# Kernel tuning notes

Measured on AMD Instinct MI355X. Metric: run time of the kernel, lower is better.

Reference implementation:

```python
import jax, jax.numpy as jnp
import numpy as np
from jax import lax


def setup_inputs() -> dict:
    key = jax.random.key(0)
    k1, k2 = jax.random.split(key)
    N, dim, m = 8192, 1024, 1024
    x = jax.random.normal(k1, (N, dim), dtype=jnp.float32)
    vectors = jax.random.normal(k2, (m, dim), dtype=jnp.float32) * 0.01
    bias = jnp.zeros((dim,), dtype=jnp.float32)
    return {"x": x, "vectors": vectors, "bias": bias}


def reference(x, vectors, bias):
    # Normalize each reflection vector to unit length: [m, d]
    v_normed = vectors / jnp.linalg.norm(vectors, axis=1, keepdims=True)

    def step(out, v):
        # out: [N, d], v: [d]
        proj = out @ v                       # [N]
        out = out - 2.0 * proj[:, None] * v  # rank-1 Householder update
        return out, None

    out, _ = lax.scan(step, x, v_normed)
    return out + bias
```

## Files before the change

### kernel.cpp

```cpp
#include <hip/hip_runtime.h>
#include <hip/hip_bf16.h>

typedef __attribute__((ext_vector_type(8))) short short8;
typedef __attribute__((ext_vector_type(4))) short s16x4;
typedef __attribute__((ext_vector_type(4))) float f32x4;

static __device__ inline short f2bf(float f) {
    unsigned u = __float_as_uint(f);
    unsigned r = (u + 0x7fffu + ((u >> 16) & 1u)) >> 16;
    return (short)r;
}
static __device__ inline float bf2f(short h) {
    return __uint_as_float(((unsigned)(unsigned short)h) << 16);
}

static __device__ inline int swz32(int row, int slot) {
    return row * 32 + ((slot ^ ((row >> 1) & 3)) << 3);
}
static __device__ inline int swz64(int row, int slot) {
    return row * 64 + ((slot ^ (row & 7)) << 3);
}

__global__ __launch_bounds__(256) void k_normalize(const float* __restrict__ vec,
                                                   float* __restrict__ V, int dim) {
    int row = blockIdx.x;
    const float4* src = (const float4*)(vec + (size_t)row * dim);
    float4* dst = (float4*)(V + (size_t)row * dim);
    int nv4 = dim >> 2;
    float ss = 0.f;
    for (int i = threadIdx.x; i < nv4; i += blockDim.x) {
        float4 v = src[i];
        ss += v.x * v.x + v.y * v.y + v.z * v.z + v.w * v.w;
    }
    for (int off = 32; off; off >>= 1) ss += __shfl_down(ss, off, 64);
    __shared__ float ws_[4];
    int lane = threadIdx.x & 63, w = threadIdx.x >> 6;
    if (lane == 0) ws_[w] = ss;
    __syncthreads();
    float inv = 1.0f / sqrtf(ws_[0] + ws_[1] + ws_[2] + ws_[3]);
    for (int i = threadIdx.x; i < nv4; i += blockDim.x) {
        float4 v = src[i];
        v.x *= inv; v.y *= inv; v.z *= inv; v.w *= inv;
        dst[i] = v;
    }
}

__global__ __launch_bounds__(256) void k_split(const float* __restrict__ X,
                                               short* __restrict__ Xh,
                                               short* __restrict__ Xl, int n4) {
    for (int i = blockIdx.x * blockDim.x + threadIdx.x; i < n4; i += gridDim.x * blockDim.x) {
        float4 v = ((const float4*)X)[i];
        float f[4] = {v.x, v.y, v.z, v.w};
        s16x4 h, l;
#pragma unroll
        for (int q = 0; q < 4; ++q) {
            h[q] = f2bf(f[q]);
            l[q] = f2bf(f[q] - bf2f(h[q]));
        }
        *(s16x4*)&Xh[(size_t)i * 4] = h;
        *(s16x4*)&Xl[(size_t)i * 4] = l;
    }
}

__global__ __launch_bounds__(256) void k_cast(const float* __restrict__ X,
                                              short* __restrict__ Xh, int n4) {
    for (int i = blockIdx.x * blockDim.x + threadIdx.x; i < n4; i += gridDim.x * blockDim.x) {
        float4 v = ((const float4*)X)[i];
        float f[4] = {v.x, v.y, v.z, v.w};
        s16x4 h;
#pragma unroll
        for (int q = 0; q < 4; ++q) h[q] = f2bf(f[q]);
        *(s16x4*)&Xh[(size_t)i * 4] = h;
    }
}

__global__ __launch_bounds__(256) void k_tsplit(const float* __restrict__ X,
                                                short* __restrict__ Xth,
                                                short* __restrict__ Xtl, int R, int C) {
    __shared__ float tile[32][33];
    int c0 = blockIdx.x * 32, r0 = blockIdx.y * 32;
    int t = threadIdx.x;
    int r = t >> 3, c4 = (t & 7) * 4;
    float4 v = *(const float4*)&X[(size_t)(r0 + r) * C + c0 + c4];
    tile[r][c4 + 0] = v.x; tile[r][c4 + 1] = v.y;
    tile[r][c4 + 2] = v.z; tile[r][c4 + 3] = v.w;
    __syncthreads();
    int rr = t >> 3, cc4 = (t & 7) * 4;
    s16x4 h, l;
#pragma unroll
    for (int q = 0; q < 4; ++q) {
        float f = tile[cc4 + q][rr];
        h[q] = f2bf(f);
        l[q] = f2bf(f - bf2f(h[q]));
    }
    *(s16x4*)&Xth[(size_t)(c0 + rr) * R + r0 + cc4] = h;
    *(s16x4*)&Xtl[(size_t)(c0 + rr) * R + r0 + cc4] = l;
}

template<int MODE, int TRI>
__global__ __launch_bounds__(256) void k_nt64(
    const short* __restrict__ Ah, const short* __restrict__ Al,
    const short* __restrict__ Bh, const short* __restrict__ Bl,
    float* __restrict__ Cf, short* __restrict__ Ch, short* __restrict__ Cl,
    int K, int lda, int ldb, int ldc) {
    __shared__ short As[2][64 * 32];
    __shared__ short Bs[2][64 * 32];
    int i0 = blockIdx.y * 64, j0 = blockIdx.x * 64;
    if (TRI == 2 && j0 < i0) return;
    int KE = (TRI == 1) ? (j0 + 64) : K;
    int t = threadIdx.x, lane = t & 63, wave = t >> 6;
    int wr = wave >> 1, wc = wave & 1;
    int srow = t >> 2, slot = t & 3;
    int sofs = swz32(srow, slot);
    int gofs = slot * 8;
    f32x4 acc[2][2] = {};
    for (int k0 = 0; k0 < KE; k0 += 32) {
        __syncthreads();
        *(short8*)&As[0][sofs] = *(const short8*)&Ah[(size_t)(i0 + srow) * lda + k0 + gofs];
        *(short8*)&As[1][sofs] = *(const short8*)&Al[(size_t)(i0 + srow) * lda + k0 + gofs];
        *(short8*)&Bs[0][sofs] = *(const short8*)&Bh[(size_t)(j0 + srow) * ldb + k0 + gofs];
        *(short8*)&Bs[1][sofs] = *(const short8*)&Bl[(size_t)(j0 + srow) * ldb + k0 + gofs];
        __syncthreads();
        int g = lane >> 4;
        short8 ah[2], al2[2], bh[2], bl2[2];
#pragma unroll
        for (int i = 0; i < 2; ++i) {
            int ro = swz32(wr * 32 + i * 16 + (lane & 15), g);
            ah[i] = *(const short8*)&As[0][ro];
            al2[i] = *(const short8*)&As[1][ro];
        }
#pragma unroll
        for (int j = 0; j < 2; ++j) {
            int ro = swz32(wc * 32 + j * 16 + (lane & 15), g);
            bh[j] = *(const short8*)&Bs[0][ro];
            bl2[j] = *(const short8*)&Bs[1][ro];
        }
#pragma unroll
        for (int i = 0; i < 2; ++i)
#pragma unroll
            for (int j = 0; j < 2; ++j) {
                acc[i][j] = __builtin_amdgcn_mfma_f32_16x16x32_bf16(ah[i], bh[j], acc[i][j], 0, 0, 0);
                acc[i][j] = __builtin_amdgcn_mfma_f32_16x16x32_bf16(ah[i], bl2[j], acc[i][j], 0, 0, 0);
                acc[i][j] = __builtin_amdgcn_mfma_f32_16x16x32_bf16(al2[i], bh[j], acc[i][j], 0, 0, 0);
            }
    }
#pragma unroll
    for (int i = 0; i < 2; ++i)
#pragma unroll
        for (int j = 0; j < 2; ++j) {
            int row0 = i0 + wr * 32 + i * 16 + ((lane >> 4) << 2);
            int col = j0 + wc * 32 + j * 16 + (lane & 15);
#pragma unroll
            for (int r = 0; r < 4; ++r) {
                float v = acc[i][j][r];
                size_t idx = (size_t)(row0 + r) * ldc + col;
                if (MODE == 2) {
                    Ch[idx] = f2bf((((row0 + r) == col) ? 1.f : 0.f) - v);
                } else {
                    short h = f2bf(v);
                    short l = f2bf(v - bf2f(h));
                    Ch[idx] = h;
                    Cl[idx] = l;
                    if (MODE == 3) Cf[idx] = v;
                }
            }
        }
}

__global__ __launch_bounds__(256) void k_baseinv2(const float* __restrict__ G,
                                                  short* __restrict__ Th, short* __restrict__ Tl,
                                                  short* __restrict__ Tth, short* __restrict__ Ttl,
                                                  int m) {
    __shared__ float Rs[64 * 64];
    int d = blockIdx.x >> 4, g = blockIdx.x & 15;
    int b0 = d * 64;
    int t = threadIdx.x, lane = t & 63, wave = t >> 6;
    {
        int r = t >> 2, c00 = (t & 3) * 16;
#pragma unroll
        for (int q = 0; q < 4; ++q)
            *(float4*)&Rs[r * 64 + c00 + q * 4] =
                *(const float4*)&G[(size_t)(b0 + r) * m + b0 + c00 + q * 4];
    }
    __syncthreads();
    int c = g * 4 + wave;
    float x = 0.f;
    for (int r = c; r >= 0; --r) {
        float prod = Rs[r * 64 + lane] * x;
        float s = prod;
#pragma unroll
        for (int off = 32; off; off >>= 1) s += __shfl_xor(s, off, 64);
        if (lane == r) x = ((r == c) ? 2.f : 0.f) - 2.f * s;
    }
    short h = f2bf(x);
    short l = f2bf(x - bf2f(h));
    Th[(size_t)(b0 + lane) * m + b0 + c] = h;
    Tl[(size_t)(b0 + lane) * m + b0 + c] = l;
    Tth[(size_t)(b0 + c) * m + b0 + lane] = h;
    Ttl[(size_t)(b0 + c) * m + b0 + lane] = l;
}

template<int PHASE>
__global__ __launch_bounds__(256) void k_trimm(
    const short* __restrict__ Ah, const short* __restrict__ Al,
    const short* __restrict__ Bh, const short* __restrict__ Bl,
    short* __restrict__ C1h, short* __restrict__ C1l,
    short* __restrict__ C2h, short* __restrict__ C2l,
    int m, int s) {
    __shared__ short As[2][64 * 32];
    __shared__ short Bs[2][64 * 32];
    int p = blockIdx.z;
    int a0 = 2 * p * s, c0 = a0 + s;
    int r0 = blockIdx.y * 64, ct = blockIdx.x * 64;
    int KS = (PHASE == 1) ? 0 : r0;
    int KE = (PHASE == 1) ? (ct + 64) : s;
    size_t tbase = (size_t)p * s * s;
    int t = threadIdx.x, lane = t & 63, wave = t >> 6;
    int wr = wave >> 1, wc = wave & 1;
    int srow = t >> 2, slot = t & 3;
    int sofs = swz32(srow, slot);
    int gofs = slot * 8;
    f32x4 acc[2][2] = {};
    for (int k0 = KS; k0 < KE; k0 += 32) {
        __syncthreads();
        if (PHASE == 1) {
            *(short8*)&As[0][sofs] = *(const short8*)&Ah[(size_t)(a0 + r0 + srow) * m + c0 + k0 + gofs];
            *(short8*)&As[1][sofs] = *(const short8*)&Al[(size_t)(a0 + r0 + srow) * m + c0 + k0 + gofs];
            *(short8*)&Bs[0][sofs] = *(const short8*)&Bh[(size_t)(c0 + ct + srow) * m + c0 + k0 + gofs];
            *(short8*)&Bs[1][sofs] = *(const short8*)&Bl[(size_t)(c0 + ct + srow) * m + c0 + k0 + gofs];
        } else {
            *(short8*)&As[0][sofs] = *(const short8*)&Ah[(size_t)(a0 + r0 + srow) * m + a0 + k0 + gofs];
            *(short8*)&As[1][sofs] = *(const short8*)&Al[(size_t)(a0 + r0 + srow) * m + a0 + k0 + gofs];
            *(short8*)&Bs[0][sofs] = *(const short8*)&Bh[tbase + (size_t)(ct + srow) * s + k0 + gofs];
            *(short8*)&Bs[1][sofs] = *(const short8*)&Bl[tbase + (size_t)(ct + srow) * s + k0 + gofs];
        }
        __syncthreads();
        int g = lane >> 4;
        short8 ah[2], al2[2], bh[2], bl2[2];
#pragma unroll
        for (int i = 0; i < 2; ++i) {
            int ro = swz32(wr * 32 + i * 16 + (lane & 15), g);
            ah[i] = *(const short8*)&As[0][ro];
            al2[i] = *(const short8*)&As[1][ro];
        }
#pragma unroll
        for (int j = 0; j < 2; ++j) {
            int ro = swz32(wc * 32 + j * 16 + (lane & 15), g);
            bh[j] = *(const short8*)&Bs[0][ro];
            bl2[j] = *(const short8*)&Bs[1][ro];
        }
#pragma unroll
        for (int i = 0; i < 2; ++i)
#pragma unroll
            for (int j = 0; j < 2; ++j) {
                acc[i][j] = __builtin_amdgcn_mfma_f32_16x16x32_bf16(ah[i], bh[j], acc[i][j], 0, 0, 0);
                acc[i][j] = __builtin_amdgcn_mfma_f32_16x16x32_bf16(ah[i], bl2[j], acc[i][j], 0, 0, 0);
                acc[i][j] = __builtin_amdgcn_mfma_f32_16x16x32_bf16(al2[i], bh[j], acc[i][j], 0, 0, 0);
            }
    }
#pragma unroll
    for (int i = 0; i < 2; ++i)
#pragma unroll
        for (int j = 0; j < 2; ++j) {
            int row0 = r0 + wr * 32 + i * 16 + ((lane >> 4) << 2);
            int col = ct + wc * 32 + j * 16 + (lane & 15);
#pragma unroll
            for (int r = 0; r < 4; ++r) {
                if (PHASE == 1) {
                    float v = acc[i][j][r];
                    short h = f2bf(v);
                    short l = f2bf(v - bf2f(h));
                    size_t idx = tbase + (size_t)col * s + row0 + r;
                    C1h[idx] = h;
                    C1l[idx] = l;
                } else {
                    float v = -acc[i][j][r];
                    short h = f2bf(v);
                    short l = f2bf(v - bf2f(h));
                    int R = a0 + row0 + r, Cc = c0 + col;
                    C1h[(size_t)R * m + Cc] = h;
                    C1l[(size_t)R * m + Cc] = l;
                    C2h[(size_t)Cc * m + R] = h;
                    C2l[(size_t)Cc * m + R] = l;
                }
            }
        }
}

__global__ __launch_bounds__(256) void k_apply3(const short* __restrict__ xh,
                                                const short* __restrict__ Qt,
                                                const float* __restrict__ bias,
                                                float* __restrict__ out, int dim) {
    __shared__ short As[128 * 64];
    __shared__ short Bs[128 * 64];
    int m0 = blockIdx.y * 128, n0 = blockIdx.x * 128;
    int t = threadIdx.x, lane = t & 63, wave = t >> 6;
    int wr = wave >> 1, wc = wave & 1;
    int sr = lane >> 3;
    int sslot = (lane & 7) ^ (sr & 7);
    f32x4 acc[4][4] = {};
    for (int k0 = 0; k0 < dim; k0 += 64) {
        __syncthreads();
#pragma unroll
        for (int q = 0; q < 4; ++q) {
            int rg = wave * 4 + q;
            int row = rg * 8 + sr;
            const short* gA = &xh[(size_t)(m0 + row) * dim + k0 + sslot * 8];
            const short* gB = &Qt[(size_t)(n0 + row) * dim + k0 + sslot * 8];
            __builtin_amdgcn_global_load_lds(
                (const __attribute__((address_space(1))) void*)gA,
                (__attribute__((address_space(3))) void*)&As[rg * 8 * 64], 16, 0, 0);
            __builtin_amdgcn_global_load_lds(
                (const __attribute__((address_space(1))) void*)gB,
                (__attribute__((address_space(3))) void*)&Bs[rg * 8 * 64], 16, 0, 0);
        }
        __syncthreads();
#pragma unroll
        for (int kk = 0; kk < 2; ++kk) {
            int g = kk * 4 + (lane >> 4);
            short8 af[4], bf_[4];
#pragma unroll
            for (int i = 0; i < 4; ++i)
                af[i] = *(const short8*)&As[swz64(wr * 64 + i * 16 + (lane & 15), g)];
#pragma unroll
            for (int j = 0; j < 4; ++j)
                bf_[j] = *(const short8*)&Bs[swz64(wc * 64 + j * 16 + (lane & 15), g)];
#pragma unroll
            for (int i = 0; i < 4; ++i)
#pragma unroll
                for (int j = 0; j < 4; ++j)
                    acc[i][j] = __builtin_amdgcn_mfma_f32_16x16x32_bf16(af[i], bf_[j], acc[i][j], 0, 0, 0);
        }
    }
#pragma unroll
    for (int i = 0; i < 4; ++i)
#pragma unroll
        for (int j = 0; j < 4; ++j) {
            int row = m0 + wr * 64 + i * 16 + (lane >> 4) * 4;
            int col = n0 + wc * 64 + j * 16 + (lane & 15);
            float b = bias[col];
#pragma unroll
            for (int r = 0; r < 4; ++r)
                out[(size_t)(row + r) * dim + col] = acc[i][j][r] + b;
        }
}

extern "C" void kernel_launch(void* const* d_in, const int* in_sizes, int n_in,
                              void* d_out, int out_size, void* d_ws, size_t ws_size,
                              hipStream_t stream) {
    const float* x = (const float*)d_in[0];
    const float* vec = (const float*)d_in[1];
    const float* bias = (const float*)d_in[2];
    float* out = (float*)d_out;

    int dim = in_sizes[2];
    int m = in_sizes[1] / dim;
    int n = in_sizes[0] / dim;

    const size_t MD = (size_t)m * dim;
    const size_t MM = (size_t)m * m;

    char* cur = (char*)d_ws;
    auto alloc_f = [&](size_t nelem) { float* p = (float*)cur; cur += nelem * 4; return p; };
    auto alloc_s = [&](size_t nelem) { short* p = (short*)cur; cur += nelem * 2; return p; };
    float* V   = alloc_f(MD);
    float* G   = alloc_f(MM);
    short* Vh  = alloc_s(MD);
    short* Vl  = alloc_s(MD);
    short* Vth = alloc_s(MD);
    short* Vtl = alloc_s(MD);
    short* Gh  = alloc_s(MM);
    short* Gl  = alloc_s(MM);
    short* Th  = alloc_s(MM);
    short* Tl  = alloc_s(MM);
    short* Tth = alloc_s(MM);
    short* Ttl = alloc_s(MM);
    short* Wh  = alloc_s(MD);
    short* Wl  = alloc_s(MD);
    short* Qt  = alloc_s((size_t)dim * dim);
    short* tmph = alloc_s(MM / 2);
    short* tmpl = alloc_s(MM / 2);
    short* xh  = alloc_s((size_t)n * dim);

    k_normalize<<<m, 256, 0, stream>>>(vec, V, dim);
    k_split<<<1024, 256, 0, stream>>>(V, Vh, Vl, (int)(MD / 4));
    k_tsplit<<<dim3(dim / 32, m / 32), 256, 0, stream>>>(V, Vth, Vtl, m, dim);

    k_nt64<3, 2><<<dim3(m / 64, m / 64), 256, 0, stream>>>(Vh, Vl, Vh, Vl, G, Gh, Gl,
                                                           dim, dim, dim, m);
    k_baseinv2<<<(m / 64) * 16, 256, 0, stream>>>(G, Th, Tl, Tth, Ttl, m);
    for (int s = 64; s < m; s <<= 1) {
        dim3 g(s / 64, s / 64, m / (2 * s));
        k_trimm<1><<<g, 256, 0, stream>>>(Gh, Gl, Tth, Ttl, tmph, tmpl, nullptr, nullptr, m, s);
        k_trimm<2><<<g, 256, 0, stream>>>(Th, Tl, tmph, tmpl, Th, Tl, Tth, Ttl, m, s);
    }

    k_nt64<1, 1><<<dim3(m / 64, dim / 64), 256, 0, stream>>>(Vth, Vtl, Tth, Ttl, nullptr, Wh, Wl,
                                                             m, m, m, m);
    k_nt64<2, 0><<<dim3(dim / 64, dim / 64), 256, 0, stream>>>(Vth, Vtl, Wh, Wl, nullptr, Qt, nullptr,
                                                               m, m, m, dim);

    k_cast<<<2048, 256, 0, stream>>>(x, xh, (int)((size_t)n * dim / 4));
    k_apply3<<<dim3(dim / 128, n / 128), 256, 0, stream>>>(xh, Qt, bias, out, dim);
}
```

Baseline: 178.9 us.

## Fuse prep kernels, double-buffer GEMM loads, add fused tree level, swizzle apply grid

Merges normalize, split and transposed split into one prep kernel. The small GEMM and the final apply GEMM become double-buffered, using global_load_lds prefetch of the next K tile with explicit waitcnt and barriers. A new fp32 kernel computes the first level of the triangular-inverse tree in one launch, replacing two trimm launches. The apply grid is remapped in a chunked order for cache locality. The aim is to cut launch overhead and memory stalls, at the cost of more LDS and fragile manual waitcnt counts.

```diff
diff --git a/kernel.cpp b/kernel.cpp
--- a/kernel.cpp
+++ b/kernel.cpp
@@ -21,44 +21,57 @@
     return row * 64 + ((slot ^ (row & 7)) << 3);
 }
 
-__global__ __launch_bounds__(256) void k_normalize(const float* __restrict__ vec,
-                                                   float* __restrict__ V, int dim) {
-    int row = blockIdx.x;
-    const float4* src = (const float4*)(vec + (size_t)row * dim);
-    float4* dst = (float4*)(V + (size_t)row * dim);
-    int nv4 = dim >> 2;
+__global__ __launch_bounds__(256) void k_prep(const float* __restrict__ vec,
+                                              short* __restrict__ Vh, short* __restrict__ Vl,
+                                              short* __restrict__ Vth, short* __restrict__ Vtl,
+                                              int m, int dim) {
+    __shared__ float ps[32][9];
+    __shared__ float invs[32];
+    __shared__ float tile[32][33];
+    int r0 = blockIdx.x * 32;
+    int t = threadIdx.x;
+    int r = t >> 3, seg = t & 7;
+    const float* src = vec + (size_t)(r0 + r) * dim + seg * 128;
     float ss = 0.f;
-    for (int i = threadIdx.x; i < nv4; i += blockDim.x) {
-        float4 v = src[i];
+#pragma unroll 8
+    for (int i = 0; i < 32; ++i) {
+        float4 v = *(const float4*)&src[i * 4];
         ss += v.x * v.x + v.y * v.y + v.z * v.z + v.w * v.w;
     }
-    for (int off = 32; off; off >>= 1) ss += __shfl_down(ss, off, 64);
-    __shared__ float ws_[4];
-    int lane = threadIdx.x & 63, w = threadIdx.x >> 6;
-    if (lane == 0) ws_[w] = ss;
+    ps[r][seg] = ss;
     __syncthreads();
-    float inv = 1.0f / sqrtf(ws_[0] + ws_[1] + ws_[2] + ws_[3]);
-    for (int i = threadIdx.x; i < nv4; i += blockDim.x) {
-        float4 v = src[i];
-        v.x *= inv; v.y *= inv; v.z *= inv; v.w *= inv;
-        dst[i] = v;
-    }
-}
-
-__global__ __launch_bounds__(256) void k_split(const float* __restrict__ X,
-                                               short* __restrict__ Xh,
-                                               short* __restrict__ Xl, int n4) {
-    for (int i = blockIdx.x * blockDim.x + threadIdx.x; i < n4; i += gridDim.x * blockDim.x) {
-        float4 v = ((const float4*)X)[i];
-        float f[4] = {v.x, v.y, v.z, v.w};
+    if (t < 32) {
+        float s = 0.f;
+#pragma unroll
+        for (int q = 0; q < 8; ++q) s += ps[t][q];
+        invs[t] = 1.0f / sqrtf(s);
+    }
+    __syncthreads();
+    float inv = invs[r];
+    int c4 = (t & 7) * 4;
+    for (int ct = 0; ct < dim / 32; ++ct) {
+        float4 v = *(const float4*)&vec[(size_t)(r0 + r) * dim + ct * 32 + c4];
+        float f[4] = {v.x * inv, v.y * inv, v.z * inv, v.w * inv};
         s16x4 h, l;
 #pragma unroll
         for (int q = 0; q < 4; ++q) {
             h[q] = f2bf(f[q]);
             l[q] = f2bf(f[q] - bf2f(h[q]));
-        }
-        *(s16x4*)&Xh[(size_t)i * 4] = h;
-        *(s16x4*)&Xl[(size_t)i * 4] = l;
+            tile[r][c4 + q] = f[q];
+        }
+        *(s16x4*)&Vh[(size_t)(r0 + r) * dim + ct * 32 + c4] = h;
+        *(s16x4*)&Vl[(size_t)(r0 + r) * dim + ct * 32 + c4] = l;
+        __syncthreads();
+        s16x4 th, tl;
+#pragma unroll
+        for (int q = 0; q < 4; ++q) {
+            float ff = tile[c4 + q][r];
+            th[q] = f2bf(ff);
+            tl[q] = f2bf(ff - bf2f(th[q]));
+        }
+        *(s16x4*)&Vth[(size_t)(ct * 32 + r) * m + r0 + c4] = th;
+        *(s16x4*)&Vtl[(size_t)(ct * 32 + r) * m + r0 + c4] = tl;
+        __syncthreads();
     }
 }
 
@@ -74,66 +87,61 @@
     }
 }
 
-__global__ __launch_bounds__(256) void k_tsplit(const float* __restrict__ X,
-                                                short* __restrict__ Xth,
-                                                short* __restrict__ Xtl, int R, int C) {
-    __shared__ float tile[32][33];
-    int c0 = blockIdx.x * 32, r0 = blockIdx.y * 32;
-    int t = threadIdx.x;
-    int r = t >> 3, c4 = (t & 7) * 4;
-    float4 v = *(const float4*)&X[(size_t)(r0 + r) * C + c0 + c4];
-    tile[r][c4 + 0] = v.x; tile[r][c4 + 1] = v.y;
-    tile[r][c4 + 2] = v.z; tile[r][c4 + 3] = v.w;
-    __syncthreads();
-    int rr = t >> 3, cc4 = (t & 7) * 4;
-    s16x4 h, l;
-#pragma unroll
-    for (int q = 0; q < 4; ++q) {
-        float f = tile[cc4 + q][rr];
-        h[q] = f2bf(f);
-        l[q] = f2bf(f - bf2f(h[q]));
-    }
-    *(s16x4*)&Xth[(size_t)(c0 + rr) * R + r0 + cc4] = h;
-    *(s16x4*)&Xtl[(size_t)(c0 + rr) * R + r0 + cc4] = l;
-}
-
 template<int MODE, int TRI>
-__global__ __launch_bounds__(256) void k_nt64(
+__global__ __launch_bounds__(256) void k_nt64g(
     const short* __restrict__ Ah, const short* __restrict__ Al,
     const short* __restrict__ Bh, const short* __restrict__ Bl,
     float* __restrict__ Cf, short* __restrict__ Ch, short* __restrict__ Cl,
     int K, int lda, int ldb, int ldc) {
-    __shared__ short As[2][64 * 32];
-    __shared__ short Bs[2][64 * 32];
+    __shared__ short As[2][2][64 * 32];
+    __shared__ short Bs[2][2][64 * 32];
     int i0 = blockIdx.y * 64, j0 = blockIdx.x * 64;
     if (TRI == 2 && j0 < i0) return;
     int KE = (TRI == 1) ? (j0 + 64) : K;
     int t = threadIdx.x, lane = t & 63, wave = t >> 6;
     int wr = wave >> 1, wc = wave & 1;
-    int srow = t >> 2, slot = t & 3;
-    int sofs = swz32(srow, slot);
-    int gofs = slot * 8;
+    int srow = wave * 16 + (lane >> 2);
+    int sslot = (lane & 3) ^ ((lane >> 3) & 3);
+    const short* gAh = &Ah[(size_t)(i0 + srow) * lda + sslot * 8];
+    const short* gAl = &Al[(size_t)(i0 + srow) * lda + sslot * 8];
+    const short* gBh = &Bh[(size_t)(j0 + srow) * ldb + sslot * 8];
+    const short* gBl = &Bl[(size_t)(j0 + srow) * ldb + sslot * 8];
+    auto stage = [&](int buf, int k0) {
+        __builtin_amdgcn_global_load_lds((const __attribute__((address_space(1))) void*)&gAh[k0],
+            (__attribute__((address_space(3))) void*)&As[buf][0][wave * 512], 16, 0, 0);
+        __builtin_amdgcn_global_load_lds((const __attribute__((address_space(1))) void*)&gAl[k0],
+            (__attribute__((address_space(3))) void*)&As[buf][1][wave * 512], 16, 0, 0);
+        __builtin_amdgcn_global_load_lds((const __attribute__((address_space(1))) void*)&gBh[k0],
+            (__attribute__((address_space(3))) void*)&Bs[buf][0][wave * 512], 16, 0, 0);
+        __builtin_amdgcn_global_load_lds((const __attribute__((address_space(1))) void*)&gBl[k0],
+            (__attribute__((address_space(3))) void*)&Bs[buf][1][wave * 512], 16, 0, 0);
+    };
+    int nIter = KE >> 5;
+    stage(0, 0);
     f32x4 acc[2][2] = {};
-    for (int k0 = 0; k0 < KE; k0 += 32) {
-        __syncthreads();
-        *(short8*)&As[0][sofs] = *(const short8*)&Ah[(size_t)(i0 + srow) * lda + k0 + gofs];
-        *(short8*)&As[1][sofs] = *(const short8*)&Al[(size_t)(i0 + srow) * lda + k0 + gofs];
-        *(short8*)&Bs[0][sofs] = *(const short8*)&Bh[(size_t)(j0 + srow) * ldb + k0 + gofs];
-        *(short8*)&Bs[1][sofs] = *(const short8*)&Bl[(size_t)(j0 + srow) * ldb + k0 + gofs];
-        __syncthreads();
+    for (int it = 0; it < nIter; ++it) {
+        int c = it & 1;
+        if (it + 1 < nIter) {
+            stage(c ^ 1, (it + 1) << 5);
+            asm volatile("s_waitcnt vmcnt(4)" ::: "memory");
+        } else {
+            asm volatile("s_waitcnt vmcnt(0)" ::: "memory");
+        }
+        __builtin_amdgcn_s_barrier();
+        __builtin_amdgcn_sched_barrier(0);
         int g = lane >> 4;
         short8 ah[2], al2[2], bh[2], bl2[2];
 #pragma unroll
         for (int i = 0; i < 2; ++i) {
             int ro = swz32(wr * 32 + i * 16 + (lane & 15), g);
-            ah[i] = *(const short8*)&As[0][ro];
-            al2[i] = *(const short8*)&As[1][ro];
+            ah[i] = *(const short8*)&As[c][0][ro];
+            al2[i] = *(const short8*)&As[c][1][ro];
         }
 #pragma unroll
         for (int j = 0; j < 2; ++j) {
             int ro = swz32(wc * 32 + j * 16 + (lane & 15), g);
-            bh[j] = *(const short8*)&Bs[0][ro];
-            bl2[j] = *(const short8*)&Bs[1][ro];
+            bh[j] = *(const short8*)&Bs[c][0][ro];
+            bl2[j] = *(const short8*)&Bs[c][1][ro];
         }
 #pragma unroll
         for (int i = 0; i < 2; ++i)
@@ -143,6 +151,8 @@
                 acc[i][j] = __builtin_amdgcn_mfma_f32_16x16x32_bf16(ah[i], bl2[j], acc[i][j], 0, 0, 0);
                 acc[i][j] = __builtin_amdgcn_mfma_f32_16x16x32_bf16(al2[i], bh[j], acc[i][j], 0, 0, 0);
             }
+        asm volatile("s_waitcnt lgkmcnt(0)" ::: "memory");
+        __builtin_amdgcn_s_barrier();
     }
 #pragma unroll
     for (int i = 0; i < 2; ++i)
@@ -198,6 +208,82 @@
     Tl[(size_t)(b0 + lane) * m + b0 + c] = l;
     Tth[(size_t)(b0 + c) * m + b0 + lane] = h;
     Ttl[(size_t)(b0 + c) * m + b0 + lane] = l;
+}
+
+__global__ __launch_bounds__(256) void k_tree64f(const float* __restrict__ G,
+                                                 short* __restrict__ Th, short* __restrict__ Tl,
+                                                 short* __restrict__ Tth, short* __restrict__ Ttl,
+                                                 int m) {
+    __shared__ float Gb[64 * 65];
+    __shared__ float Ai[64 * 65];
+    __shared__ float Ci[64 * 64];
+    __shared__ float Tm[64 * 64];
+    int p = blockIdx.x;
+    int a0 = p * 128, c0 = a0 + 64;
+    int t = threadIdx.x;
+    {
+        int r = t >> 2, c00 = (t & 3) * 16;
+#pragma unroll
+        for (int q = 0; q < 4; ++q) {
+            *(float4*)&Gb[r * 65 + c00 + q * 4] =
+                *(const float4*)&G[(size_t)(a0 + r) * m + c0 + c00 + q * 4];
+            s16x4 ha = *(const s16x4*)&Th[(size_t)(a0 + r) * m + a0 + c00 + q * 4];
+            s16x4 la = *(const s16x4*)&Tl[(size_t)(a0 + r) * m + a0 + c00 + q * 4];
+            s16x4 hc = *(const s16x4*)&Th[(size_t)(c0 + r) * m + c0 + c00 + q * 4];
+            s16x4 lc = *(const s16x4*)&Tl[(size_t)(c0 + r) * m + c0 + c00 + q * 4];
+#pragma unroll
+            for (int e = 0; e < 4; ++e) {
+                Ai[r * 65 + c00 + q * 4 + e] = bf2f(ha[e]) + bf2f(la[e]);
+                Ci[r * 64 + c00 + q * 4 + e] = bf2f(hc[e]) + bf2f(lc[e]);
+            }
+        }
+    }
+    __syncthreads();
+    int tx = t & 15, ty = t >> 4;
+    float acc[4][4] = {};
+#pragma unroll 4
+    for (int k = 0; k < 64; ++k) {
+        float av[4], bv[4];
+#pragma unroll
+        for (int i = 0; i < 4; ++i) av[i] = Gb[(ty * 4 + i) * 65 + k];
+#pragma unroll
+        for (int j = 0; j < 4; ++j) bv[j] = Ci[k * 64 + tx * 4 + j];
+#pragma unroll
+        for (int i = 0; i < 4; ++i)
+#pragma unroll
+            for (int j = 0; j < 4; ++j) acc[i][j] += av[i] * bv[j];
+    }
+#pragma unroll
+    for (int i = 0; i < 4; ++i)
+#pragma unroll
+        for (int j = 0; j < 4; ++j) Tm[(ty * 4 + i) * 64 + tx * 4 + j] = acc[i][j];
+    __syncthreads();
+    float acc2[4][4] = {};
+#pragma unroll 4
+    for (int k = 0; k < 64; ++k) {
+        float av[4], bv[4];
+#pragma unroll
+        for (int i = 0; i < 4; ++i) av[i] = Ai[(ty * 4 + i) * 65 + k];
+#pragma unroll
+        for (int j = 0; j < 4; ++j) bv[j] = Tm[k * 64 + tx * 4 + j];
+#pragma unroll
+        for (int i = 0; i < 4; ++i)
+#pragma unroll
+            for (int j = 0; j < 4; ++j) acc2[i][j] += av[i] * bv[j];
+    }
+#pragma unroll
+    for (int i = 0; i < 4; ++i)
+#pragma unroll
+        for (int j = 0; j < 4; ++j) {
+            float v = -acc2[i][j];
+            short h = f2bf(v);
+            short l = f2bf(v - bf2f(h));
+            int R = a0 + ty * 4 + i, C = c0 + tx * 4 + j;
+            Th[(size_t)R * m + C] = h;
+            Tl[(size_t)R * m + C] = l;
+            Tth[(size_t)C * m + R] = h;
+            Ttl[(size_t)C * m + R] = l;
+        }
 }
 
 template<int PHASE>
@@ -287,20 +373,22 @@
         }
 }
 
-__global__ __launch_bounds__(256) void k_apply3(const short* __restrict__ xh,
+__global__ __launch_bounds__(256) void k_apply4(const short* __restrict__ xh,
                                                 const short* __restrict__ Qt,
                                                 const float* __restrict__ bias,
                                                 float* __restrict__ out, int dim) {
-    __shared__ short As[128 * 64];
-    __shared__ short Bs[128 * 64];
-    int m0 = blockIdx.y * 128, n0 = blockIdx.x * 128;
+    __shared__ short As[2][128 * 64];
+    __shared__ short Bs[2][128 * 64];
+    int nwg = gridDim.x * gridDim.y;
+    int flat = blockIdx.y * gridDim.x + blockIdx.x;
+    int cpx = nwg >> 3;
+    int L = (flat & 7) * cpx + (flat >> 3);
+    int m0 = (L / gridDim.x) * 128, n0 = (L % gridDim.x) * 128;
     int t = threadIdx.x, lane = t & 63, wave = t >> 6;
     int wr = wave >> 1, wc = wave & 1;
     int sr = lane >> 3;
     int sslot = (lane & 7) ^ (sr & 7);
-    f32x4 acc[4][4] = {};
-    for (int k0 = 0; k0 < dim; k0 += 64) {
-        __syncthreads();
+    auto stage = [&](int buf, int k0) {
 #pragma unroll
         for (int q = 0; q < 4; ++q) {
             int rg = wave * 4 + q;
@@ -309,28 +397,43 @@
             const short* gB = &Qt[(size_t)(n0 + row) * dim + k0 + sslot * 8];
             __builtin_amdgcn_global_load_lds(
                 (const __attribute__((address_space(1))) void*)gA,
-                (__attribute__((address_space(3))) void*)&As[rg * 8 * 64], 16, 0, 0);
+                (__attribute__((address_space(3))) void*)&As[buf][rg * 8 * 64], 16, 0, 0);
             __builtin_amdgcn_global_load_lds(
                 (const __attribute__((address_space(1))) void*)gB,
-                (__attribute__((address_space(3))) void*)&Bs[rg * 8 * 64], 16, 0, 0);
-        }
-        __syncthreads();
+                (__attribute__((address_space(3))) void*)&Bs[buf][rg * 8 * 64], 16, 0, 0);
+        }
+    };
+    int nIter = dim >> 6;
+    stage(0, 0);
+    f32x4 acc[4][4] = {};
+    for (int it = 0; it < nIter; ++it) {
+        int c = it & 1;
+        if (it + 1 < nIter) {
+            stage(c ^ 1, (it + 1) << 6);
+            asm volatile("s_waitcnt vmcnt(8)" ::: "memory");
+        } else {
+            asm volatile("s_waitcnt vmcnt(0)" ::: "memory");
+        }
+        __builtin_amdgcn_s_barrier();
+        __builtin_amdgcn_sched_barrier(0);
 #pragma unroll
         for (int kk = 0; kk < 2; ++kk) {
             int g = kk * 4 + (lane >> 4);
             short8 af[4], bf_[4];
 #pragma unroll
             for (int i = 0; i < 4; ++i)
-                af[i] = *(const short8*)&As[swz64(wr * 64 + i * 16 + (lane & 15), g)];
+                af[i] = *(const short8*)&As[c][swz64(wr * 64 + i * 16 + (lane & 15), g)];
 #pragma unroll
             for (int j = 0; j < 4; ++j)
-                bf_[j] = *(const short8*)&Bs[swz64(wc * 64 + j * 16 + (lane & 15), g)];
+                bf_[j] = *(const short8*)&Bs[c][swz64(wc * 64 + j * 16 + (lane & 15), g)];
 #pragma unroll
             for (int i = 0; i < 4; ++i)
 #pragma unroll
                 for (int j = 0; j < 4; ++j)
                     acc[i][j] = __builtin_amdgcn_mfma_f32_16x16x32_bf16(af[i], bf_[j], acc[i][j], 0, 0, 0);
         }
+        asm volatile("s_waitcnt lgkmcnt(0)" ::: "memory");
+        __builtin_amdgcn_s_barrier();
     }
 #pragma unroll
     for (int i = 0; i < 4; ++i)
@@ -363,7 +466,6 @@
     char* cur = (char*)d_ws;
     auto alloc_f = [&](size_t nelem) { float* p = (float*)cur; cur += nelem * 4; return p; };
     auto alloc_s = [&](size_t nelem) { short* p = (short*)cur; cur += nelem * 2; return p; };
-    float* V   = alloc_f(MD);
     float* G   = alloc_f(MM);
     short* Vh  = alloc_s(MD);
     short* Vl  = alloc_s(MD);
@@ -382,24 +484,23 @@
     short* tmpl = alloc_s(MM / 2);
     short* xh  = alloc_s((size_t)n * dim);
 
-    k_normalize<<<m, 256, 0, stream>>>(vec, V, dim);
-    k_split<<<1024, 256, 0, stream>>>(V, Vh, Vl, (int)(MD / 4));
-    k_tsplit<<<dim3(dim / 32, m / 32), 256, 0, stream>>>(V, Vth, Vtl, m, dim);
-
-    k_nt64<3, 2><<<dim3(m / 64, m / 64), 256, 0, stream>>>(Vh, Vl, Vh, Vl, G, Gh, Gl,
-                                                           dim, dim, dim, m);
+    k_prep<<<m / 32, 256, 0, stream>>>(vec, Vh, Vl, Vth, Vtl, m, dim);
+
+    k_nt64g<3, 2><<<dim3(m / 64, m / 64), 256, 0, stream>>>(Vh, Vl, Vh, Vl, G, Gh, Gl,
+                                                            dim, dim, dim, m);
     k_baseinv2<<<(m / 64) * 16, 256, 0, stream>>>(G, Th, Tl, Tth, Ttl, m);
-    for (int s = 64; s < m; s <<= 1) {
+    k_tree64f<<<m / 128, 256, 0, stream>>>(G, Th, Tl, Tth, Ttl, m);
+    for (int s = 128; s < m; s <<= 1) {
         dim3 g(s / 64, s / 64, m / (2 * s));
         k_trimm<1><<<g, 256, 0, stream>>>(Gh, Gl, Tth, Ttl, tmph, tmpl, nullptr, nullptr, m, s);
         k_trimm<2><<<g, 256, 0, stream>>>(Th, Tl, tmph, tmpl, Th, Tl, Tth, Ttl, m, s);
     }
 
-    k_nt64<1, 1><<<dim3(m / 64, dim / 64), 256, 0, stream>>>(Vth, Vtl, Tth, Ttl, nullptr, Wh, Wl,
-                                                             m, m, m, m);
-    k_nt64<2, 0><<<dim3(dim / 64, dim / 64), 256, 0, stream>>>(Vth, Vtl, Wh, Wl, nullptr, Qt, nullptr,
-                                                               m, m, m, dim);
+    k_nt64g<1, 1><<<dim3(m / 64, dim / 64), 256, 0, stream>>>(Vth, Vtl, Tth, Ttl, nullptr, Wh, Wl,
+                                                              m, m, m, m);
+    k_nt64g<2, 0><<<dim3(dim / 64, dim / 64), 256, 0, stream>>>(Vth, Vtl, Wh, Wl, nullptr, Qt, nullptr,
+                                                                m, m, m, dim);
 
     k_cast<<<2048, 256, 0, stream>>>(x, xh, (int)((size_t)n * dim / 4));
-    k_apply3<<<dim3(dim / 128, n / 128), 256, 0, stream>>>(xh, Qt, bias, out, dim);
-}
+    k_apply4<<<dim3(dim / 128, n / 128), 256, 0, stream>>>(xh, Qt, bias, out, dim);
+}
```

Result: slower. 187.4 us (+4.8%).
